# Kernel optimization log

Hardware: AMD Instinct MI355X
Metric: run time of the kernel (lower is better)

Reference implementation:

```python
import jax, jax.numpy as jnp
import numpy as np

B, P, E, F = 65536, 16, 32, 64  # batch, n_patches, n_edges, feature_dim


def setup_inputs() -> dict:
    key = jax.random.key(0)
    k1, k2 = jax.random.split(key, 2)
    node_sections = jax.random.normal(k1, (B, P, F), dtype=jnp.float32)
    incidence = (jax.random.normal(k2, (E, P), dtype=jnp.float32) * 0.1)
    # torch init: each sheaf map = eye(feature_dim) * 0.1, stacked -> [E, F, F]
    sheaf_maps = jnp.tile((jnp.eye(F, dtype=jnp.float32) * 0.1)[None], (E, 1, 1))
    damping = jnp.asarray(0.1, dtype=jnp.float32)
    return {"node_sections": node_sections, "incidence": incidence,
            "sheaf_maps": sheaf_maps, "damping": damping}


def reference(node_sections, incidence, sheaf_maps, damping):
    # Coboundary: weighted[b,e,:] = sum_p incidence[e,p] * sections[b,p,:];
    # then per-edge matmul with sheaf_maps[e].
    weighted = jnp.einsum('ep,bpf->bef', incidence, node_sections)
    coboundary = jnp.einsum('bef,efg->beg', weighted, sheaf_maps)
    # Laplacian diffusion: delta^T delta [P,P] applied over patch dim.
    dTd = jnp.einsum('ep,eq->pq', incidence, incidence)
    diffused = node_sections - damping * jnp.einsum('pq,bqf->bpf', dTd, node_sections)
    # H1 energy proxy: per-edge L2 norm, averaged over edges -> [B]
    h1_norm = jnp.linalg.norm(coboundary, axis=-1).mean(axis=-1)
    return diffused, h1_norm
```

## Files before the change

### kernel.cpp

```cpp
#include <hip/hip_runtime.h>
#include <hip/hip_bf16.h>

typedef __attribute__((ext_vector_type(8))) short short8;
typedef __attribute__((ext_vector_type(4))) float floatx4;

#define NB 65536
#define STS 18
#define WES 68
#define WBS 1092

static __device__ __forceinline__ ushort f2bf(float x) {
  union { float f; unsigned u; } v; v.f = x;
  unsigned r = v.u + 0x7FFFu + ((v.u >> 16) & 1u);
  return (ushort)(r >> 16);
}

__global__ void sheaf_prep(const float* __restrict__ inc,
                           const float* __restrict__ M,
                           const float* __restrict__ damp,
                           ushort* __restrict__ Mt,
                           ushort* __restrict__ L) {
  const int bid = blockIdx.x, tid = threadIdx.x;
  if (bid < 32) {
    const float* Me = M + (bid << 12);
    ushort* Mte = Mt + (bid << 12);
    for (int i = tid; i < 4096; i += 256) {
      int g = i >> 6, f = i & 63;
      Mte[(g << 6) + f] = f2bf(Me[(f << 6) + g]);
    }
  } else {
    for (int i = tid; i < 1024; i += 256) {
      int e = i >> 5, col = i & 31;
      L[(e << 5) + col] = (col < 16) ? f2bf(inc[(e << 4) + col]) : (ushort)0;
    }
    float d = damp[0];
    int p = tid >> 4, q = tid & 15;
    float s = 0.f;
    for (int e = 0; e < 32; ++e)
      s += inc[(e << 4) + p] * inc[(e << 4) + q];
    float a = ((p == q) ? 1.f : 0.f) - d * s;
    L[((32 + p) << 5) + q] = f2bf(a);
    L[((32 + p) << 5) + 16 + q] = (ushort)0;
  }
}

__global__ __launch_bounds__(256, 2) void sheaf_main(
    const float* __restrict__ S,
    const ushort* __restrict__ Mt,
    const ushort* __restrict__ L,
    float* __restrict__ out) {
  __shared__ ushort st[1024 * STS];
  __shared__ ushort wl[16 * WBS];
  __shared__ float h1s[4][16];

  const int tid = threadIdx.x;
  const int lane = tid & 63;
  const int w = tid >> 6;
  const int quad = lane >> 4;
  const int l15 = lane & 15;

  {
    const float4* gS = (const float4*)S + (size_t)blockIdx.x * 4096;
    #pragma unroll
    for (int i = 0; i < 16; ++i) {
      int v = tid + (i << 8);
      float4 raw = gS[v];
      int b = v >> 8, p = (v >> 4) & 15, fv = v & 15;
      int base = ((b << 6) + (fv << 2)) * STS + p;
      st[base]           = f2bf(raw.x);
      st[base + STS]     = f2bf(raw.y);
      st[base + 2 * STS] = f2bf(raw.z);
      st[base + 3 * STS] = f2bf(raw.w);
    }
  }

  short8 aL0 = *(const short8*)(L + (l15) * 32 + (quad << 3));
  short8 aL1 = *(const short8*)(L + (16 + l15) * 32 + (quad << 3));
  short8 aLp = *(const short8*)(L + (32 + l15) * 32 + (quad << 3));

  __syncthreads();

  float hp = 0.f;

  for (int ec = 0; ec < 2; ++ec) {
    short8 aE = ec ? aL1 : aL0;
    for (int t = 0; t < 16; ++t) {
      int ctile = (w << 4) + t;
      int c = (ctile << 4) + l15;
      short8 bf;
      {
        union { short8 v; unsigned wds[4]; } u;
        if (quad < 2) {
          const unsigned* row = (const unsigned*)(st + c * STS);
          int o = quad << 2;
          u.wds[0] = row[o];     u.wds[1] = row[o + 1];
          u.wds[2] = row[o + 2]; u.wds[3] = row[o + 3];
        } else {
          u.wds[0] = 0u; u.wds[1] = 0u; u.wds[2] = 0u; u.wds[3] = 0u;
        }
        bf = u.v;
      }
      floatx4 acc = {0.f, 0.f, 0.f, 0.f};
      acc = __builtin_amdgcn_mfma_f32_16x16x32_bf16(aE, bf, acc, 0, 0, 0);
      int b = c >> 6, f = c & 63;
      int wbase = b * WBS + f;
      #pragma unroll
      for (int r = 0; r < 4; ++r) {
        int eloc = (quad << 2) + r;
        wl[wbase + eloc * WES] = f2bf(acc[r]);
      }
      if (ec == 0) {
        floatx4 accD = {0.f, 0.f, 0.f, 0.f};
        accD = __builtin_amdgcn_mfma_f32_16x16x32_bf16(aLp, bf, accD, 0, 0, 0);
        size_t obase = ((size_t)blockIdx.x * 16 + (size_t)b) * 1024 + (size_t)f;
        #pragma unroll
        for (int r = 0; r < 4; ++r) {
          int p = (quad << 2) + r;
          out[obase + p * 64] = accD[r];
        }
      }
    }
    __syncthreads();

    #pragma unroll
    for (int i = 0; i < 4; ++i) {
      int eloc = (w << 2) + i;
      int e = (ec << 4) + eloc;
      const ushort* MtE = Mt + (e << 12);
      float ss = 0.f;
      #pragma unroll
      for (int gt = 0; gt < 4; ++gt) {
        floatx4 acc = {0.f, 0.f, 0.f, 0.f};
        #pragma unroll
        for (int ks = 0; ks < 2; ++ks) {
          short8 af = *(const short8*)(MtE + (((gt << 4) + l15) << 6) + (ks << 5) + (quad << 3));
          union { short8 v; uint2 u2[2]; } ub;
          const uint2* pw = (const uint2*)(wl + l15 * WBS + eloc * WES + (ks << 5) + (quad << 3));
          ub.u2[0] = pw[0]; ub.u2[1] = pw[1];
          acc = __builtin_amdgcn_mfma_f32_16x16x32_bf16(af, ub.v, acc, 0, 0, 0);
        }
        ss += acc[0]*acc[0] + acc[1]*acc[1] + acc[2]*acc[2] + acc[3]*acc[3];
      }
      ss += __shfl_xor(ss, 16);
      ss += __shfl_xor(ss, 32);
      hp += sqrtf(ss);
    }
    __syncthreads();
  }

  if (lane < 16) h1s[w][l15] = hp;
  __syncthreads();
  if (tid < 16) {
    float tsum = (h1s[0][tid] + h1s[1][tid] + h1s[2][tid] + h1s[3][tid]) * (1.f / 32.f);
    out[(size_t)NB * 1024 + (size_t)blockIdx.x * 16 + tid] = tsum;
  }
}

extern "C" void kernel_launch(void* const* d_in, const int* in_sizes, int n_in,
                              void* d_out, int out_size, void* d_ws, size_t ws_size,
                              hipStream_t stream) {
  const float* S   = (const float*)d_in[0];
  const float* inc = (const float*)d_in[1];
  const float* M   = (const float*)d_in[2];
  const float* dmp = (const float*)d_in[3];
  float* out = (float*)d_out;

  ushort* Mt = (ushort*)d_ws;
  ushort* L  = Mt + 131072;

  sheaf_prep<<<33, 256, 0, stream>>>(inc, M, dmp, Mt, L);
  sheaf_main<<<NB / 16, 256, 0, stream>>>(S, Mt, L, out);
}
```

Measured before the change: 529.0 us.

## Halve batch per block, swap MFMA operand roles for vectorized stores

Each block now handles 8 batch items instead of 16, which halves shared memory and raises the launch-bounds occupancy target from 2 to 4 blocks. The MFMA operand order is swapped so each lane's accumulator holds 4 consecutive features. That lets the diffused output go out as float4 stores and the weighted intermediate be packed into uint2 LDS writes. The global load is restructured into per-thread strided gathers with packed bf16 stores, and the second-stage B fragments are hoisted out of the gt loop. In exchange, the lanes 8-15 in the second stage duplicate work, and the input loads become strided scalar reads instead of float4.

```diff
diff --git a/kernel.cpp b/kernel.cpp
--- a/kernel.cpp
+++ b/kernel.cpp
@@ -1,18 +1,21 @@
 #include <hip/hip_runtime.h>
-#include <hip/hip_bf16.h>
 
 typedef __attribute__((ext_vector_type(8))) short short8;
 typedef __attribute__((ext_vector_type(4))) float floatx4;
 
 #define NB 65536
+#define BPB 8
 #define STS 18
 #define WES 68
-#define WBS 1092
+#define WBS 1096
 
 static __device__ __forceinline__ ushort f2bf(float x) {
   union { float f; unsigned u; } v; v.f = x;
   unsigned r = v.u + 0x7FFFu + ((v.u >> 16) & 1u);
   return (ushort)(r >> 16);
+}
+static __device__ __forceinline__ unsigned pk2(float a, float b) {
+  return (unsigned)f2bf(a) | ((unsigned)f2bf(b) << 16);
 }
 
 __global__ void sheaf_prep(const float* __restrict__ inc,
@@ -44,80 +47,70 @@
   }
 }
 
-__global__ __launch_bounds__(256, 2) void sheaf_main(
+__global__ __launch_bounds__(256, 4) void sheaf_main(
     const float* __restrict__ S,
     const ushort* __restrict__ Mt,
     const ushort* __restrict__ L,
     float* __restrict__ out) {
-  __shared__ ushort st[1024 * STS];
-  __shared__ ushort wl[16 * WBS];
-  __shared__ float h1s[4][16];
+  __shared__ ushort st[512 * STS];
+  __shared__ ushort wl[BPB * WBS];
+  __shared__ float h1s[4][BPB];
 
-  const int tid = threadIdx.x;
+  const int tid  = threadIdx.x;
   const int lane = tid & 63;
-  const int w = tid >> 6;
+  const int w    = tid >> 6;
   const int quad = lane >> 4;
-  const int l15 = lane & 15;
+  const int l15  = lane & 15;
 
-  {
-    const float4* gS = (const float4*)S + (size_t)blockIdx.x * 4096;
+  #pragma unroll
+  for (int k = 0; k < 2; ++k) {
+    int c = tid + (k << 8);
+    int b = c >> 6, f = c & 63;
+    const float* src = S + (size_t)blockIdx.x * (BPB * 1024) + b * 1024 + f;
+    float v[16];
     #pragma unroll
-    for (int i = 0; i < 16; ++i) {
-      int v = tid + (i << 8);
-      float4 raw = gS[v];
-      int b = v >> 8, p = (v >> 4) & 15, fv = v & 15;
-      int base = ((b << 6) + (fv << 2)) * STS + p;
-      st[base]           = f2bf(raw.x);
-      st[base + STS]     = f2bf(raw.y);
-      st[base + 2 * STS] = f2bf(raw.z);
-      st[base + 3 * STS] = f2bf(raw.w);
-    }
+    for (int p = 0; p < 16; ++p) v[p] = src[p << 6];
+    unsigned* dst = (unsigned*)st + c * 9;
+    #pragma unroll
+    for (int pp = 0; pp < 8; ++pp) dst[pp] = pk2(v[2 * pp], v[2 * pp + 1]);
   }
 
-  short8 aL0 = *(const short8*)(L + (l15) * 32 + (quad << 3));
-  short8 aL1 = *(const short8*)(L + (16 + l15) * 32 + (quad << 3));
-  short8 aLp = *(const short8*)(L + (32 + l15) * 32 + (quad << 3));
+  short8 bL0 = *(const short8*)(L + (l15) * 32 + (quad << 3));
+  short8 bL1 = *(const short8*)(L + (16 + l15) * 32 + (quad << 3));
+  short8 bLp = *(const short8*)(L + (32 + l15) * 32 + (quad << 3));
 
   __syncthreads();
 
   float hp = 0.f;
 
   for (int ec = 0; ec < 2; ++ec) {
-    short8 aE = ec ? aL1 : aL0;
-    for (int t = 0; t < 16; ++t) {
-      int ctile = (w << 4) + t;
-      int c = (ctile << 4) + l15;
-      short8 bf;
+    short8 bE = ec ? bL1 : bL0;
+    for (int t = 0; t < 8; ++t) {
+      int cb = ((w << 3) + t) << 4;
+      short8 aS;
       {
-        union { short8 v; unsigned wds[4]; } u;
+        union { short8 v; unsigned d[4]; } u;
         if (quad < 2) {
-          const unsigned* row = (const unsigned*)(st + c * STS);
-          int o = quad << 2;
-          u.wds[0] = row[o];     u.wds[1] = row[o + 1];
-          u.wds[2] = row[o + 2]; u.wds[3] = row[o + 3];
+          const unsigned* row = (const unsigned*)st + (cb + l15) * 9 + (quad << 2);
+          u.d[0] = row[0]; u.d[1] = row[1]; u.d[2] = row[2]; u.d[3] = row[3];
         } else {
-          u.wds[0] = 0u; u.wds[1] = 0u; u.wds[2] = 0u; u.wds[3] = 0u;
+          u.d[0] = 0u; u.d[1] = 0u; u.d[2] = 0u; u.d[3] = 0u;
         }
-        bf = u.v;
+        aS = u.v;
       }
-      floatx4 acc = {0.f, 0.f, 0.f, 0.f};
-      acc = __builtin_amdgcn_mfma_f32_16x16x32_bf16(aE, bf, acc, 0, 0, 0);
-      int b = c >> 6, f = c & 63;
-      int wbase = b * WBS + f;
-      #pragma unroll
-      for (int r = 0; r < 4; ++r) {
-        int eloc = (quad << 2) + r;
-        wl[wbase + eloc * WES] = f2bf(acc[r]);
-      }
+      int b  = cb >> 6;
+      int fb = (cb & 63) + (quad << 2);
+      floatx4 accW = {0.f, 0.f, 0.f, 0.f};
+      accW = __builtin_amdgcn_mfma_f32_16x16x32_bf16(aS, bE, accW, 0, 0, 0);
+      uint2 pkv;
+      pkv.x = pk2(accW[0], accW[1]);
+      pkv.y = pk2(accW[2], accW[3]);
+      *(uint2*)(wl + b * WBS + l15 * WES + fb) = pkv;
       if (ec == 0) {
         floatx4 accD = {0.f, 0.f, 0.f, 0.f};
-        accD = __builtin_amdgcn_mfma_f32_16x16x32_bf16(aLp, bf, accD, 0, 0, 0);
-        size_t obase = ((size_t)blockIdx.x * 16 + (size_t)b) * 1024 + (size_t)f;
-        #pragma unroll
-        for (int r = 0; r < 4; ++r) {
-          int p = (quad << 2) + r;
-          out[obase + p * 64] = accD[r];
-        }
+        accD = __builtin_amdgcn_mfma_f32_16x16x32_bf16(aS, bLp, accD, 0, 0, 0);
+        float4 o; o.x = accD[0]; o.y = accD[1]; o.z = accD[2]; o.w = accD[3];
+        *(float4*)(out + ((size_t)blockIdx.x * BPB + b) * 1024 + l15 * 64 + fb) = o;
       }
     }
     __syncthreads();
@@ -127,18 +120,25 @@
       int eloc = (w << 2) + i;
       int e = (ec << 4) + eloc;
       const ushort* MtE = Mt + (e << 12);
+      short8 bW0, bW1;
+      {
+        const ushort* base = wl + (l15 & 7) * WBS + eloc * WES + (quad << 3);
+        union { short8 v; uint2 d[2]; } u0, u1;
+        u0.d[0] = *(const uint2*)(base);
+        u0.d[1] = *(const uint2*)(base + 4);
+        u1.d[0] = *(const uint2*)(base + 32);
+        u1.d[1] = *(const uint2*)(base + 36);
+        bW0 = u0.v; bW1 = u1.v;
+      }
       float ss = 0.f;
       #pragma unroll
       for (int gt = 0; gt < 4; ++gt) {
+        const ushort* ma = MtE + (((gt << 4) + l15) << 6) + (quad << 3);
+        short8 a0 = *(const short8*)(ma);
+        short8 a1 = *(const short8*)(ma + 32);
         floatx4 acc = {0.f, 0.f, 0.f, 0.f};
-        #pragma unroll
-        for (int ks = 0; ks < 2; ++ks) {
-          short8 af = *(const short8*)(MtE + (((gt << 4) + l15) << 6) + (ks << 5) + (quad << 3));
-          union { short8 v; uint2 u2[2]; } ub;
-          const uint2* pw = (const uint2*)(wl + l15 * WBS + eloc * WES + (ks << 5) + (quad << 3));
-          ub.u2[0] = pw[0]; ub.u2[1] = pw[1];
-          acc = __builtin_amdgcn_mfma_f32_16x16x32_bf16(af, ub.v, acc, 0, 0, 0);
-        }
+        acc = __builtin_amdgcn_mfma_f32_16x16x32_bf16(a0, bW0, acc, 0, 0, 0);
+        acc = __builtin_amdgcn_mfma_f32_16x16x32_bf16(a1, bW1, acc, 0, 0, 0);
         ss += acc[0]*acc[0] + acc[1]*acc[1] + acc[2]*acc[2] + acc[3]*acc[3];
       }
       ss += __shfl_xor(ss, 16);
@@ -148,11 +148,11 @@
     __syncthreads();
   }
 
-  if (lane < 16) h1s[w][l15] = hp;
+  if (lane < 8) h1s[w][lane] = hp;
   __syncthreads();
-  if (tid < 16) {
-    float tsum = (h1s[0][tid] + h1s[1][tid] + h1s[2][tid] + h1s[3][tid]) * (1.f / 32.f);
-    out[(size_t)NB * 1024 + (size_t)blockIdx.x * 16 + tid] = tsum;
+  if (tid < 8) {
+    float s = (h1s[0][tid] + h1s[1][tid] + h1s[2][tid] + h1s[3][tid]) * (1.f / 32.f);
+    out[(size_t)NB * 1024 + (size_t)blockIdx.x * BPB + tid] = s;
   }
 }
 
@@ -169,5 +169,5 @@
   ushort* L  = Mt + 131072;
 
   sheaf_prep<<<33, 256, 0, stream>>>(inc, M, dmp, Mt, L);
-  sheaf_main<<<NB / 16, 256, 0, stream>>>(S, Mt, L, out);
+  sheaf_main<<<NB / BPB, 256, 0, stream>>>(S, Mt, L, out);
 }
```

Result: slower. 604.0 us (+14.2%).
